# Performance work log

Hardware: AMD Instinct MI355X
Metric: run time of the kernel (lower is better)

Reference implementation:

```python
import jax, jax.numpy as jnp
import numpy as np

HIDDEN = 2048
N_HEADS = 32
N_KV_HEADS = 8
HEAD_DIM = HIDDEN // N_HEADS  # 64
ROPE_BASE = 10000.0
B, S = 2, 2048
NEG_INF = -1e9


def rotate_half(x):
    x1, x2 = jnp.split(x, 2, axis=-1)
    return jnp.concatenate((-x2, x1), axis=-1)


def rope_cos_sin(seq_len, head_dim, base, dtype):
    inv_freq = 1.0 / (base ** (jnp.arange(0, head_dim, 2, dtype=jnp.float32) / head_dim))
    pos = jnp.arange(seq_len, dtype=jnp.float32)
    freqs = jnp.outer(pos, inv_freq)              # [S, D/2]
    emb = jnp.concatenate((freqs, freqs), axis=-1)  # [S, D]
    return jnp.cos(emb).astype(dtype)[None, None], jnp.sin(emb).astype(dtype)[None, None]


def setup_inputs() -> dict:
    key = jax.random.key(0)
    ks = jax.random.split(key, 5)
    hidden_states = jax.random.normal(ks[0], (B, S, HIDDEN), dtype=jnp.float32)
    # causal additive mask, Llama-style
    causal = jnp.tril(jnp.ones((S, S), dtype=bool))
    attention_mask = jnp.where(causal, 0.0, NEG_INF).astype(jnp.float32)
    attention_mask = jnp.broadcast_to(attention_mask[None, None], (B, 1, S, S))
    sc = 1.0 / np.sqrt(HIDDEN)
    Wq = jax.random.normal(ks[1], (HIDDEN, HIDDEN), dtype=jnp.float32) * sc
    Wk = jax.random.normal(ks[2], (N_KV_HEADS * HEAD_DIM, HIDDEN), dtype=jnp.float32) * sc
    Wv = jax.random.normal(ks[3], (N_KV_HEADS * HEAD_DIM, HIDDEN), dtype=jnp.float32) * sc
    Wo = jax.random.normal(ks[4], (HIDDEN, HIDDEN), dtype=jnp.float32) * sc
    return {"hidden_states": hidden_states, "attention_mask": attention_mask,
            "Wq": Wq, "Wk": Wk, "Wv": Wv, "Wo": Wo}


def reference(hidden_states, attention_mask, Wq, Wk, Wv, Wo):
    b, s, _ = hidden_states.shape
    groups = N_HEADS // N_KV_HEADS
    # projections (torch Linear: x @ W.T)
    q = (hidden_states @ Wq.T).reshape(b, s, N_HEADS, HEAD_DIM).transpose(0, 2, 1, 3)      # [b,H,s,d]
    k = (hidden_states @ Wk.T).reshape(b, s, N_KV_HEADS, HEAD_DIM).transpose(0, 2, 1, 3)   # [b,Hk,s,d]
    v = (hidden_states @ Wv.T).reshape(b, s, N_KV_HEADS, HEAD_DIM).transpose(0, 2, 1, 3)
    cos, sin = rope_cos_sin(s, HEAD_DIM, ROPE_BASE, hidden_states.dtype)
    q = q * cos + rotate_half(q) * sin
    k = k * cos + rotate_half(k) * sin
    # GQA without materializing repeated K/V: view q as [b, Hk, g, s, d]
    qg = q.reshape(b, N_KV_HEADS, groups, s, HEAD_DIM)
    scores = jnp.einsum('bhgqd,bhkd->bhgqk', qg, k) / np.sqrt(HEAD_DIM)  # [b,Hk,g,s,s]
    scores = scores + attention_mask[:, :, None]                          # mask [b,1,1,s,s]
    probs = jax.nn.softmax(scores.astype(jnp.float32), axis=-1).astype(q.dtype)
    attn = jnp.einsum('bhgqk,bhkd->bhgqd', probs, v)                      # [b,Hk,g,s,d]
    attn = attn.reshape(b, N_HEADS, s, HEAD_DIM).transpose(0, 2, 1, 3).reshape(b, s, HIDDEN)
    return attn @ Wo.T
```

## Files before the change

kernel.cpp:

```cpp
#include <hip/hip_runtime.h>
#include <math.h>

#define HID 2048
#define NH 32
#define NKV 8
#define HD 64
#define BB 2
#define SS 2048
#define MTOT (BB * SS)

typedef __bf16 bf16;
typedef __bf16 bf16x8 __attribute__((ext_vector_type(8)));
typedef __bf16 bf16x4 __attribute__((ext_vector_type(4)));
typedef float f32x4 __attribute__((ext_vector_type(4)));

#define MFMA16(a, b, c) __builtin_amdgcn_mfma_f32_16x16x32_bf16((a), (b), (c), 0, 0, 0)

__device__ __forceinline__ void load_lds16(const void* g, void* l) {
  __builtin_amdgcn_global_load_lds((const __attribute__((address_space(1))) void*)g,
                                   (__attribute__((address_space(3))) void*)l, 16, 0, 0);
}

#define FENCE() asm volatile("" ::: "memory")
#define SYNC_VM(N) do { FENCE(); \
  asm volatile("s_waitcnt vmcnt(" #N ") lgkmcnt(0)" ::: "memory"); \
  __builtin_amdgcn_s_barrier(); FENCE(); } while (0)

__global__ void cvt_all(const float* __restrict__ hs, const float* __restrict__ Wq,
                        const float* __restrict__ Wk, const float* __restrict__ Wv,
                        const float* __restrict__ Wo,
                        bf16* __restrict__ A_b, bf16* __restrict__ Wq_b,
                        bf16* __restrict__ Wk_b, bf16* __restrict__ Wv_b,
                        bf16* __restrict__ Wo_b) {
  int bid = blockIdx.x;
  const float* src;
  bf16* dst;
  if (bid < 8192)       { src = hs; dst = A_b; }
  else if (bid < 12288) { src = Wq; dst = Wq_b; bid -= 8192; }
  else if (bid < 13312) { src = Wk; dst = Wk_b; bid -= 12288; }
  else if (bid < 14336) { src = Wv; dst = Wv_b; bid -= 13312; }
  else                  { src = Wo; dst = Wo_b; bid -= 14336; }
  int i = (bid * 256 + threadIdx.x) * 4;
  float4 v = *(const float4*)(src + i);
  bf16x4 o;
  o[0] = (bf16)v.x; o[1] = (bf16)v.y; o[2] = (bf16)v.z; o[3] = (bf16)v.w;
  *(bf16x4*)(dst + i) = o;
}

__device__ __forceinline__ void gemm_core256x128(const char* Agc, const char* Bgc,
                                                 char* lds, f32x4 (&acc)[4][4]) {
  constexpr int ABYTES = 16384;
  constexpr int BUFB = 24576;
  constexpr int NT = HID / 32;

  const int tid = threadIdx.x;
  const int w = tid >> 6, lane = tid & 63;
  const int l16 = lane & 15, quad = lane >> 4;
  const int wr = w >> 1, wc = w & 1;
  const int wb = w * 1024;

  const int cu = (tid & 7) ^ ((tid >> 3) & 7);
  const int srcR0 = 2 * (tid >> 3) + (cu >> 2);
  const int srcC = (cu & 3) * 16;
  const char* gA = Agc + (size_t)srcR0 * (HID * 2) + srcC;
  const char* gB = Bgc + (size_t)srcR0 * (HID * 2) + srcC;

  const int acg16 = ((((l16 & 1) << 2) | quad) ^ ((l16 >> 1) & 7)) * 16;
  const int aoff = (wr * 32 + (l16 >> 1)) * 128 + acg16;
  const int boff = ABYTES + (wc * 32 + (l16 >> 1)) * 128 + acg16;

#pragma unroll
  for (int t0 = 0; t0 < 2; ++t0) {
    char* lb = lds + t0 * BUFB;
    load_lds16(gA + t0 * 64, lb + wb);
    load_lds16(gA + (size_t)128 * (HID * 2) + t0 * 64, lb + 8192 + wb);
    load_lds16(gB + t0 * 64, lb + ABYTES + wb);
  }

  char* cur = lds;
  char* stg = lds + 2 * BUFB;
  for (int kt = 0; kt < NT; ++kt) {
    SYNC_VM(3);
    const int ks = (kt + 2 < NT) ? (kt + 2) * 64 : (NT - 1) * 64;

    load_lds16(gA + ks, stg + wb);
    load_lds16(gA + (size_t)128 * (HID * 2) + ks, stg + 8192 + wb);
    load_lds16(gB + ks, stg + ABYTES + wb);
    FENCE();

    bf16x8 af[4], bfr[4];
#pragma unroll
    for (int ni = 0; ni < 4; ++ni)
      bfr[ni] = *(const bf16x8*)(cur + boff + ni * 1024);
#pragma unroll
    for (int mi = 0; mi < 4; ++mi)
      af[mi] = *(const bf16x8*)(cur + aoff + mi * 1024);
    __builtin_amdgcn_s_setprio(1);
#pragma unroll
    for (int mi = 0; mi < 4; ++mi)
#pragma unroll
      for (int ni = 0; ni < 4; ++ni)
        acc[mi][ni] = MFMA16(af[mi], bfr[ni], acc[mi][ni]);
    __builtin_amdgcn_s_setprio(0);

    cur = (cur == lds + 2 * BUFB) ? lds : cur + BUFB;
    stg = (stg == lds + 2 * BUFB) ? lds : stg + BUFB;
  }
  asm volatile("s_waitcnt vmcnt(0)" ::: "memory");
}

#define QSCALE 0.1803368801f
#define L2B 0.4152410118f
__global__ __launch_bounds__(512, 4) void gemm_qkv(const bf16* __restrict__ A,
                                                   const bf16* __restrict__ Wq,
                                                   const bf16* __restrict__ Wk,
                                                   const bf16* __restrict__ Wv,
                                                   bf16* __restrict__ Qb,
                                                   bf16* __restrict__ Kb,
                                                   bf16* __restrict__ Vt) {
  __shared__ __align__(16) char lds[3 * 24576];
  const int tileM = blockIdx.x * 256;
  const int n0 = blockIdx.y * 128;
  const bf16* Wp;
  int mode;
  if (n0 < HID) { Wp = Wq + (size_t)n0 * HID; mode = 0; }
  else if (n0 < HID + 512) { Wp = Wk + (size_t)(n0 - HID) * HID; mode = 1; }
  else { Wp = Wv + (size_t)(n0 - HID - 512) * HID; mode = 2; }

  f32x4 acc[4][4];
#pragma unroll
  for (int i = 0; i < 4; ++i)
#pragma unroll
    for (int j = 0; j < 4; ++j) acc[i][j] = (f32x4){0.f, 0.f, 0.f, 0.f};

  gemm_core256x128((const char*)(A + (size_t)tileM * HID), (const char*)Wp, lds, acc);

  const int tid = threadIdx.x;
  const int w = tid >> 6, lane = tid & 63;
  const int l16 = lane & 15, quad = lane >> 4;
  const int wr = w >> 1, wc = w & 1;
  const int mbase = tileM + wr * 64;
  const int cb = n0 + wc * 64;

  if (mode == 2) {
#pragma unroll
    for (int mi = 0; mi < 4; ++mi)
#pragma unroll
      for (int ni = 0; ni < 4; ++ni)
#pragma unroll
        for (int r = 0; r < 4; ++r) {
          int grow = mbase + mi * 16 + quad * 4 + r;
          int b = grow >> 11, spos = grow & (SS - 1);
          int nv = cb + ni * 16 + l16 - (HID + 512);
          Vt[(((size_t)(b * NKV + (nv >> 6))) * HD + (nv & 63)) * SS + spos] =
              (bf16)acc[mi][ni][r];
        }
  } else {
    const float inv0 = __builtin_amdgcn_exp2f(-(float)l16 * L2B);
    const float inv1 = __builtin_amdgcn_exp2f(-(float)(l16 + 16) * L2B);
#pragma unroll
    for (int mi = 0; mi < 4; ++mi) {
#pragma unroll
      for (int r = 0; r < 4; ++r) {
        int grow = mbase + mi * 16 + quad * 4 + r;
        int b = grow >> 11, spos = grow & (SS - 1);
        float sn0, cs0, sn1, cs1;
        sincosf((float)spos * inv0, &sn0, &cs0);
        sincosf((float)spos * inv1, &sn1, &cs1);
        float a0 = acc[mi][0][r], a1 = acc[mi][1][r];
        float a2 = acc[mi][2][r], a3 = acc[mi][3][r];
        float o0 = a0 * cs0 - a2 * sn0;
        float o2 = a2 * cs0 + a0 * sn0;
        float o1 = a1 * cs1 - a3 * sn1;
        float o3 = a3 * cs1 + a1 * sn1;
        if (mode == 0) {
          bf16* qp = Qb + (size_t)grow * HID + cb + l16;
          qp[0]  = (bf16)(o0 * QSCALE);
          qp[16] = (bf16)(o1 * QSCALE);
          qp[32] = (bf16)(o2 * QSCALE);
          qp[48] = (bf16)(o3 * QSCALE);
        } else {
          int kvh = (cb - HID) >> 6;
          bf16* kp = Kb + ((size_t)(b * NKV + kvh) * SS + spos) * HD + l16;
          kp[0]  = (bf16)o0;
          kp[16] = (bf16)o1;
          kp[32] = (bf16)o2;
          kp[48] = (bf16)o3;
        }
      }
    }
  }
}

__global__ __launch_bounds__(512, 4) void gemm_out(const bf16* __restrict__ A,
                                                   const bf16* __restrict__ Wo,
                                                   float* __restrict__ out) {
  __shared__ __align__(16) char lds[3 * 24576];
  const int tileM = blockIdx.x * 256;
  const int n0 = blockIdx.y * 128;
  f32x4 acc[4][4];
#pragma unroll
  for (int i = 0; i < 4; ++i)
#pragma unroll
    for (int j = 0; j < 4; ++j) acc[i][j] = (f32x4){0.f, 0.f, 0.f, 0.f};

  gemm_core256x128((const char*)(A + (size_t)tileM * HID),
                   (const char*)(Wo + (size_t)n0 * HID), lds, acc);

  const int tid = threadIdx.x;
  const int w = tid >> 6, lane = tid & 63;
  const int l16 = lane & 15, quad = lane >> 4;
  const int wr = w >> 1, wc = w & 1;
#pragma unroll
  for (int mi = 0; mi < 4; ++mi)
#pragma unroll
    for (int ni = 0; ni < 4; ++ni)
#pragma unroll
      for (int r = 0; r < 4; ++r) {
        int grow = tileM + wr * 64 + mi * 16 + quad * 4 + r;
        int gcol = n0 + wc * 64 + ni * 16 + l16;
        out[(size_t)grow * HID + gcol] = acc[mi][ni][r];
      }
}

#define PSTR 72
__global__ __launch_bounds__(256, 3) void attn(const bf16* __restrict__ Qb,
                                               const bf16* __restrict__ Kb,
                                               const bf16* __restrict__ Vt,
                                               bf16* __restrict__ Ctx) {
  __shared__ bf16 Ktile[2][64 * 64];
  __shared__ bf16 Vtile[2][64 * 64];
  __shared__ bf16 Pbuf[4][16 * PSTR];
  const int tid = threadIdx.x;
  const int w = tid >> 6, lane = tid & 63;
  const int l16 = lane & 15, quad = lane >> 4;
  const int bh = blockIdx.y, b = bh >> 5, h = bh & 31, kvh = h >> 2;
  bf16* Pw = &Pbuf[w][0];
  const char* Kslice = (const char*)(Kb + ((size_t)(b * NKV + kvh)) * SS * HD);
  const char* Vslice = (const char*)(Vt + ((size_t)(b * NKV + kvh)) * HD * SS);
  const int qrel = w * 16 + l16;

  const int srow = (lane >> 3) & 7;
  const int pchunk = ((lane & 7) ^ srow) << 4;
  const int so = ((quad ^ (l16 & 7)) << 4);
  const int so2 = so ^ 64;

  const int qtA = (int)blockIdx.x;

  int cur = 0;
  {
#pragma unroll
    for (int i = 0; i < 2; ++i) {
      const int r = w * 16 + i * 8 + srow;
      load_lds16(Kslice + (size_t)r * 128 + pchunk,
                 (char*)Ktile[0] + (w * 16 + i * 8) * 128);
      load_lds16(Vslice + (size_t)r * 4096 + pchunk,
                 (char*)Vtile[0] + (w * 16 + i * 8) * 128);
    }
  }

  for (int t = 0; t < 2; ++t) {
    const int qt = t ? (31 - qtA) : qtA;
    const int q = qt * 64 + qrel;

    const bf16* Qp = Qb + ((size_t)(b * SS + q)) * HID + h * HD + quad * 8;
    bf16x8 qb0 = *(const bf16x8*)Qp;
    bf16x8 qb1 = *(const bf16x8*)(Qp + 32);

    float l = 0.f;
    f32x4 oacc[4];
#pragma unroll
    for (int d = 0; d < 4; ++d) oacc[d] = (f32x4){0.f, 0.f, 0.f, 0.f};

    for (int kt = 0; kt <= qt; ++kt) {
      __syncthreads();

      const bool have_next = (kt < qt) || (t == 0);
      if (have_next) {
        const int nkb = (kt < qt) ? (kt + 1) * 64 : 0;
        const int nb = cur ^ 1;
#pragma unroll
        for (int i = 0; i < 2; ++i) {
          const int r = w * 16 + i * 8 + srow;
          load_lds16(Kslice + (size_t)(nkb + r) * 128 + pchunk,
                     (char*)Ktile[nb] + (w * 16 + i * 8) * 128);
          load_lds16(Vslice + (size_t)r * 4096 + (size_t)nkb * 2 + pchunk,
                     (char*)Vtile[nb] + (w * 16 + i * 8) * 128);
        }
      }

      const char* Kc = (const char*)Ktile[cur] + l16 * 128;
      const char* Vc = (const char*)Vtile[cur] + l16 * 128;
      const bool diag = (kt == qt);

#pragma unroll
      for (int nt = 0; nt < 4; ++nt) {
        bf16x8 kf0 = *(const bf16x8*)(Kc + nt * 2048 + so);
        bf16x8 kf1 = *(const bf16x8*)(Kc + nt * 2048 + so2);
        f32x4 s = {0.f, 0.f, 0.f, 0.f};
        s = MFMA16(kf0, qb0, s);
        s = MFMA16(kf1, qb1, s);
        bf16x4 pk;
        if (diag) {
          const int krel = nt * 16 + quad * 4;
#pragma unroll
          for (int r = 0; r < 4; ++r) {
            float p = (krel + r > qrel) ? 0.f : __builtin_amdgcn_exp2f(s[r]);
            l += p;
            pk[r] = (bf16)p;
          }
        } else {
#pragma unroll
          for (int r = 0; r < 4; ++r) {
            float p = __builtin_amdgcn_exp2f(s[r]);
            l += p;
            pk[r] = (bf16)p;
          }
        }
        *(bf16x4*)&Pw[l16 * PSTR + nt * 16 + quad * 4] = pk;
      }

      bf16x8 p0 = *(const bf16x8*)&Pw[l16 * PSTR + quad * 8];
      bf16x8 p1 = *(const bf16x8*)&Pw[l16 * PSTR + 32 + quad * 8];
#pragma unroll
      for (int dn = 0; dn < 4; ++dn) {
        bf16x8 v0 = *(const bf16x8*)(Vc + dn * 2048 + so);
        bf16x8 v1 = *(const bf16x8*)(Vc + dn * 2048 + so2);
        oacc[dn] = MFMA16(v0, p0, oacc[dn]);
        oacc[dn] = MFMA16(v1, p1, oacc[dn]);
      }
      cur ^= 1;
    }

    l += __shfl_xor(l, 16);
    l += __shfl_xor(l, 32);
    const float inv = 1.0f / l;
    bf16* Cp = Ctx + ((size_t)(b * SS + q)) * HID + h * HD + quad * 4;
#pragma unroll
    for (int dn = 0; dn < 4; ++dn) {
      bf16x4 ov;
#pragma unroll
      for (int r = 0; r < 4; ++r) ov[r] = (bf16)(oacc[dn][r] * inv);
      *(bf16x4*)(Cp + dn * 16) = ov;
    }
  }
}

extern "C" void kernel_launch(void* const* d_in, const int* in_sizes, int n_in,
                              void* d_out, int out_size, void* d_ws, size_t ws_size,
                              hipStream_t stream) {
  const float* hs = (const float*)d_in[0];
  const float* Wq = (const float*)d_in[2];
  const float* Wk = (const float*)d_in[3];
  const float* Wv = (const float*)d_in[4];
  const float* Wo = (const float*)d_in[5];

  char* ws = (char*)d_ws;
  bf16* A_b  = (bf16*)(ws);
  bf16* Wq_b = (bf16*)(ws + 16777216);
  bf16* Wk_b = (bf16*)(ws + 25165824);
  bf16* Wv_b = (bf16*)(ws + 27262976);
  bf16* Wo_b = (bf16*)(ws + 29360128);
  bf16* Qb   = (bf16*)(ws + 37748736);
  bf16* Kb   = (bf16*)(ws + 54525952);
  bf16* Vt   = (bf16*)(ws + 58720256);
  bf16* Ctx  = A_b;

  cvt_all<<<18432, 256, 0, stream>>>(hs, Wq, Wk, Wv, Wo, A_b, Wq_b, Wk_b, Wv_b, Wo_b);
  gemm_qkv<<<dim3(MTOT / 256, 24), 512, 0, stream>>>(A_b, Wq_b, Wk_b, Wv_b, Qb, Kb, Vt);
  attn<<<dim3(16, BB * NH), 256, 0, stream>>>(Qb, Kb, Vt, Ctx);
  gemm_out<<<dim3(MTOT / 256, HID / 128), 512, 0, stream>>>(Ctx, Wo_b, (float*)d_out);
}
```

Before: 307.4 us.

## Process two query tiles per attention block to reuse K/V tiles

Each attention block now handles a 128-row query span (two 64-row tiles) instead of 64, so every K/V tile loaded into LDS feeds MFMAs for both query tiles. The grid is halved to 8 blocks per head, with the same front/back pairing used for causal load balance. This roughly halves K/V global and LDS traffic per unit of work. In exchange it doubles accumulator registers and the P buffer, and the first tile wastes a diagonal iteration emitting zeros, which may lower occupancy. Halving the grid also reduces the number of blocks available to fill the GPU.

```diff
diff --git a/kernel.cpp b/kernel.cpp
--- a/kernel.cpp
+++ b/kernel.cpp
@@ -230,7 +230,7 @@
                                                bf16* __restrict__ Ctx) {
   __shared__ bf16 Ktile[2][64 * 64];
   __shared__ bf16 Vtile[2][64 * 64];
-  __shared__ bf16 Pbuf[4][16 * PSTR];
+  __shared__ bf16 Pbuf[4][32 * PSTR];
   const int tid = threadIdx.x;
   const int w = tid >> 6, lane = tid & 63;
   const int l16 = lane & 15, quad = lane >> 4;
@@ -245,7 +245,7 @@
   const int so = ((quad ^ (l16 & 7)) << 4);
   const int so2 = so ^ 64;
 
-  const int qtA = (int)blockIdx.x;
+  const int xA = (int)blockIdx.x;
 
   int cur = 0;
   {
@@ -260,24 +260,31 @@
   }
 
   for (int t = 0; t < 2; ++t) {
-    const int qt = t ? (31 - qtA) : qtA;
-    const int q = qt * 64 + qrel;
-
-    const bf16* Qp = Qb + ((size_t)(b * SS + q)) * HID + h * HD + quad * 8;
-    bf16x8 qb0 = *(const bf16x8*)Qp;
-    bf16x8 qb1 = *(const bf16x8*)(Qp + 32);
-
-    float l = 0.f;
-    f32x4 oacc[4];
-#pragma unroll
-    for (int d = 0; d < 4; ++d) oacc[d] = (f32x4){0.f, 0.f, 0.f, 0.f};
-
-    for (int kt = 0; kt <= qt; ++kt) {
+    const int X = t ? (15 - xA) : xA;
+    const int qA = X * 128 + qrel;
+    const int ktmax = 2 * X + 1;
+
+    const bf16* QpA = Qb + ((size_t)(b * SS + qA)) * HID + h * HD + quad * 8;
+    bf16x8 qa0 = *(const bf16x8*)QpA;
+    bf16x8 qa1 = *(const bf16x8*)(QpA + 32);
+    const bf16* QpB = QpA + (size_t)64 * HID;
+    bf16x8 qbB0 = *(const bf16x8*)QpB;
+    bf16x8 qbB1 = *(const bf16x8*)(QpB + 32);
+
+    float lA = 0.f, lB = 0.f;
+    f32x4 oA[4], oB[4];
+#pragma unroll
+    for (int d = 0; d < 4; ++d) {
+      oA[d] = (f32x4){0.f, 0.f, 0.f, 0.f};
+      oB[d] = (f32x4){0.f, 0.f, 0.f, 0.f};
+    }
+
+    for (int kt = 0; kt <= ktmax; ++kt) {
       __syncthreads();
 
-      const bool have_next = (kt < qt) || (t == 0);
+      const bool have_next = (kt < ktmax) || (t == 0);
       if (have_next) {
-        const int nkb = (kt < qt) ? (kt + 1) * 64 : 0;
+        const int nkb = (kt < ktmax) ? (kt + 1) * 64 : 0;
         const int nb = cur ^ 1;
 #pragma unroll
         for (int i = 0; i < 2; ++i) {
@@ -291,57 +298,98 @@
 
       const char* Kc = (const char*)Ktile[cur] + l16 * 128;
       const char* Vc = (const char*)Vtile[cur] + l16 * 128;
-      const bool diag = (kt == qt);
+      const bool skipA = (kt == ktmax);
+      const bool diagA = (kt == ktmax - 1);
+      const bool diagB = (kt == ktmax);
 
 #pragma unroll
       for (int nt = 0; nt < 4; ++nt) {
         bf16x8 kf0 = *(const bf16x8*)(Kc + nt * 2048 + so);
         bf16x8 kf1 = *(const bf16x8*)(Kc + nt * 2048 + so2);
-        f32x4 s = {0.f, 0.f, 0.f, 0.f};
-        s = MFMA16(kf0, qb0, s);
-        s = MFMA16(kf1, qb1, s);
-        bf16x4 pk;
-        if (diag) {
-          const int krel = nt * 16 + quad * 4;
+        const int krel = nt * 16 + quad * 4;
+
+        bf16x4 pkA;
+        if (skipA) {
+          pkA[0] = (bf16)0.f; pkA[1] = (bf16)0.f;
+          pkA[2] = (bf16)0.f; pkA[3] = (bf16)0.f;
+        } else {
+          f32x4 s = {0.f, 0.f, 0.f, 0.f};
+          s = MFMA16(kf0, qa0, s);
+          s = MFMA16(kf1, qa1, s);
+          if (diagA) {
+#pragma unroll
+            for (int r = 0; r < 4; ++r) {
+              float p = (krel + r > qrel) ? 0.f : __builtin_amdgcn_exp2f(s[r]);
+              lA += p;
+              pkA[r] = (bf16)p;
+            }
+          } else {
+#pragma unroll
+            for (int r = 0; r < 4; ++r) {
+              float p = __builtin_amdgcn_exp2f(s[r]);
+              lA += p;
+              pkA[r] = (bf16)p;
+            }
+          }
+        }
+        *(bf16x4*)&Pw[l16 * PSTR + krel] = pkA;
+
+        f32x4 sB = {0.f, 0.f, 0.f, 0.f};
+        sB = MFMA16(kf0, qbB0, sB);
+        sB = MFMA16(kf1, qbB1, sB);
+        bf16x4 pkB;
+        if (diagB) {
 #pragma unroll
           for (int r = 0; r < 4; ++r) {
-            float p = (krel + r > qrel) ? 0.f : __builtin_amdgcn_exp2f(s[r]);
-            l += p;
-            pk[r] = (bf16)p;
+            float p = (krel + r > qrel) ? 0.f : __builtin_amdgcn_exp2f(sB[r]);
+            lB += p;
+            pkB[r] = (bf16)p;
           }
         } else {
 #pragma unroll
           for (int r = 0; r < 4; ++r) {
-            float p = __builtin_amdgcn_exp2f(s[r]);
-            l += p;
-            pk[r] = (bf16)p;
+            float p = __builtin_amdgcn_exp2f(sB[r]);
+            lB += p;
+            pkB[r] = (bf16)p;
           }
         }
-        *(bf16x4*)&Pw[l16 * PSTR + nt * 16 + quad * 4] = pk;
-      }
-
-      bf16x8 p0 = *(const bf16x8*)&Pw[l16 * PSTR + quad * 8];
-      bf16x8 p1 = *(const bf16x8*)&Pw[l16 * PSTR + 32 + quad * 8];
+        *(bf16x4*)&Pw[(16 + l16) * PSTR + krel] = pkB;
+      }
+
+      bf16x8 pA0 = *(const bf16x8*)&Pw[l16 * PSTR + quad * 8];
+      bf16x8 pA1 = *(const bf16x8*)&Pw[l16 * PSTR + 32 + quad * 8];
+      bf16x8 pB0 = *(const bf16x8*)&Pw[(16 + l16) * PSTR + quad * 8];
+      bf16x8 pB1 = *(const bf16x8*)&Pw[(16 + l16) * PSTR + 32 + quad * 8];
 #pragma unroll
       for (int dn = 0; dn < 4; ++dn) {
         bf16x8 v0 = *(const bf16x8*)(Vc + dn * 2048 + so);
         bf16x8 v1 = *(const bf16x8*)(Vc + dn * 2048 + so2);
-        oacc[dn] = MFMA16(v0, p0, oacc[dn]);
-        oacc[dn] = MFMA16(v1, p1, oacc[dn]);
+        oA[dn] = MFMA16(v0, pA0, oA[dn]);
+        oA[dn] = MFMA16(v1, pA1, oA[dn]);
+        oB[dn] = MFMA16(v0, pB0, oB[dn]);
+        oB[dn] = MFMA16(v1, pB1, oB[dn]);
       }
       cur ^= 1;
     }
 
-    l += __shfl_xor(l, 16);
-    l += __shfl_xor(l, 32);
-    const float inv = 1.0f / l;
-    bf16* Cp = Ctx + ((size_t)(b * SS + q)) * HID + h * HD + quad * 4;
+    lA += __shfl_xor(lA, 16);
+    lA += __shfl_xor(lA, 32);
+    lB += __shfl_xor(lB, 16);
+    lB += __shfl_xor(lB, 32);
+    const float invA = 1.0f / lA;
+    const float invB = 1.0f / lB;
+    bf16* CpA = Ctx + ((size_t)(b * SS + qA)) * HID + h * HD + quad * 4;
+    bf16* CpB = CpA + (size_t)64 * HID;
 #pragma unroll
     for (int dn = 0; dn < 4; ++dn) {
-      bf16x4 ov;
-#pragma unroll
-      for (int r = 0; r < 4; ++r) ov[r] = (bf16)(oacc[dn][r] * inv);
-      *(bf16x4*)(Cp + dn * 16) = ov;
+      bf16x4 ovA, ovB;
+#pragma unroll
+      for (int r = 0; r < 4; ++r) {
+        ovA[r] = (bf16)(oA[dn][r] * invA);
+        ovB[r] = (bf16)(oB[dn][r] * invB);
+      }
+      *(bf16x4*)(CpA + dn * 16) = ovA;
+      *(bf16x4*)(CpB + dn * 16) = ovB;
     }
   }
 }
@@ -368,6 +416,6 @@
 
   cvt_all<<<18432, 256, 0, stream>>>(hs, Wq, Wk, Wv, Wo, A_b, Wq_b, Wk_b, Wv_b, Wo_b);
   gemm_qkv<<<dim3(MTOT / 256, 24), 512, 0, stream>>>(A_b, Wq_b, Wk_b, Wv_b, Qb, Kb, Vt);
-  attn<<<dim3(16, BB * NH), 256, 0, stream>>>(Qb, Kb, Vt, Ctx);
+  attn<<<dim3(8, BB * NH), 256, 0, stream>>>(Qb, Kb, Vt, Ctx);
   gemm_out<<<dim3(MTOT / 256, HID / 128), 512, 0, stream>>>(Ctx, Wo_b, (float*)d_out);
 }
```

Result: faster. 298.5 us (-2.9%).
